# Performance work log

Measured on AMD Instinct MI355X. Metric: run time of the kernel, lower is better.

## Reference

```python
import jax, jax.numpy as jnp
import numpy as np

N_AGENTS = 8
STATE_DIM = 256
EMBED_DIM = 32
BATCH = 65536


def setup_inputs() -> dict:
    key = jax.random.key(0)
    ks = jax.random.split(key, 12)
    s = 1.0 / np.sqrt(STATE_DIM)
    se = 1.0 / np.sqrt(EMBED_DIM)
    return {
        "agent_qs": jax.random.normal(ks[0], (BATCH, N_AGENTS), dtype=jnp.float32),
        "states": jax.random.normal(ks[1], (BATCH, STATE_DIM), dtype=jnp.float32),
        # hyper_w_1: Linear(state_dim, embed_dim * n_agents)
        "w1_W": jax.random.uniform(ks[2], (STATE_DIM, EMBED_DIM * N_AGENTS), jnp.float32, -s, s),
        "w1_b": jax.random.uniform(ks[3], (EMBED_DIM * N_AGENTS,), jnp.float32, -s, s),
        # hyper_w_final: Linear(state_dim, embed_dim)
        "wf_W": jax.random.uniform(ks[4], (STATE_DIM, EMBED_DIM), jnp.float32, -s, s),
        "wf_b": jax.random.uniform(ks[5], (EMBED_DIM,), jnp.float32, -s, s),
        # hyper_b_1: Linear(state_dim, embed_dim)
        "b1_W": jax.random.uniform(ks[6], (STATE_DIM, EMBED_DIM), jnp.float32, -s, s),
        "b1_b": jax.random.uniform(ks[7], (EMBED_DIM,), jnp.float32, -s, s),
        # V: Linear(state_dim, embed_dim) -> ReLU -> Linear(embed_dim, 1)
        "v1_W": jax.random.uniform(ks[8], (STATE_DIM, EMBED_DIM), jnp.float32, -s, s),
        "v1_b": jax.random.uniform(ks[9], (EMBED_DIM,), jnp.float32, -s, s),
        "v2_W": jax.random.uniform(ks[10], (EMBED_DIM, 1), jnp.float32, -se, se),
        "v2_b": jax.random.uniform(ks[11], (1,), jnp.float32, -se, se),
    }


def reference(agent_qs, states, w1_W, w1_b, wf_W, wf_b, b1_W, b1_b, v1_W, v1_b, v2_W, v2_b):
    B = agent_qs.shape[0]
    # hypernet weights (abs for monotonicity)
    w1 = jnp.abs(states @ w1_W + w1_b).reshape(B, N_AGENTS, EMBED_DIM)   # [B, A, E]
    w_final = jnp.abs(states @ wf_W + wf_b)                               # [B, E]
    b1 = states @ b1_W + b1_b                                             # [B, E]
    # hidden = elu(agent_qs^T w1 + b1): [B,1,A] @ [B,A,E] -> [B,E]
    hidden = jax.nn.elu(jnp.einsum("ba,bae->be", agent_qs, w1) + b1)
    # mixed = hidden @ w_final: [B,1,E] @ [B,E,1] -> [B,1]
    mixed = jnp.sum(hidden * w_final, axis=-1, keepdims=True)             # [B, 1]
    # state value V(s)
    state_value = jax.nn.relu(states @ v1_W + v1_b) @ v2_W + v2_b         # [B, 1]
    return mixed + state_value
```

## Files before the change

kernel.cpp:

```cpp
#include <hip/hip_runtime.h>
#include <math.h>


#define NTILES 22
#define KCHUNKS 8
#define CHUNK_I4 1408

typedef __attribute__((ext_vector_type(8))) short short8;
typedef __attribute__((ext_vector_type(4))) float float4v;

__device__ __forceinline__ unsigned short f2b(float f) {
    unsigned int u = __float_as_uint(f);
    u = u + 0x7fffu + ((u >> 16) & 1u);
    return (unsigned short)(u >> 16);
}

__device__ __forceinline__ void gl2lds16(const unsigned short* g, unsigned short* l) {
    __builtin_amdgcn_global_load_lds(
        (const __attribute__((address_space(1))) unsigned int*)g,
        (__attribute__((address_space(3))) unsigned int*)l,
        16, 0, 0);
}

__device__ __forceinline__ float4v ld16_async(const float* p) {
    float4v r;
    asm volatile("global_load_dwordx4 %0, %1, off" : "=v"(r) : "v"(p));
    return r;
}

__global__ void repack_b(const float* __restrict__ w1_W,
                         const float* __restrict__ wf_W,
                         const float* __restrict__ b1_W,
                         const float* __restrict__ v1_W,
                         unsigned short* __restrict__ brep) {
    int idx = blockIdx.x * 256 + threadIdx.x;
    int lane = idx & 63;
    int tt   = idx >> 6;
    int t    = tt % 22;
    int kc   = tt / 22;
    int kbase = kc * 32 + (lane >> 4) * 8;
    int n = t * 16 + (lane & 15);
    short8 frag;
#pragma unroll
    for (int j = 0; j < 8; ++j) {
        int k = kbase + j;
        float val;
        if (n < 256)      val = w1_W[k * 256 + n];
        else if (n < 288) val = wf_W[k * 32 + (n - 256)];
        else if (n < 320) val = b1_W[k * 32 + (n - 288)];
        else              val = v1_W[k * 32 + (n - 320)];
        frag[j] = (short)f2b(val);
    }
    *(short8*)(&brep[idx * 8]) = frag;
}

__global__ void __launch_bounds__(256, 2)
qmix_main(const float* __restrict__ agent_qs,
          const float* __restrict__ states,
          const unsigned short* __restrict__ brep,
          const float* __restrict__ w1_b,
          const float* __restrict__ wf_b,
          const float* __restrict__ b1_b,
          const float* __restrict__ v1_b,
          const float* __restrict__ v2_W,
          const float* __restrict__ v2_b,
          float* __restrict__ out) {
    __shared__ __align__(16) unsigned short wlds[2][NTILES * 64 * 8];

    const int tid  = threadIdx.x;
    const int wave = tid >> 6, lane = tid & 63;
    const int quad = lane >> 4, l16 = lane & 15;
    const int r0 = blockIdx.x * 128 + wave * 32 + l16;
    const float* srow0 = states + (size_t)r0 * 256;
    const float* srow1 = srow0 + 16 * 256;

    float4v st[4];

#define ISSUE_STATES(kcv) do {                                          \
        const float* p0_ = srow0 + (kcv) * 32 + quad * 8;               \
        const float* p1_ = srow1 + (kcv) * 32 + quad * 8;               \
        st[0] = ld16_async(p0_);                                        \
        st[1] = ld16_async(p0_ + 4);                                    \
        st[2] = ld16_async(p1_);                                        \
        st[3] = ld16_async(p1_ + 4);                                    \
    } while (0)

#define ISSUE_DMA(kcv, bufv) do {                                       \
        const unsigned short* src_ = brep + (size_t)(kcv) * CHUNK_I4 * 8; \
        unsigned short* dst_ = wlds[bufv];                              \
        for (int s_ = wave; s_ < NTILES; s_ += 4)                       \
            gl2lds16(src_ + (size_t)(s_ * 64 + lane) * 8, dst_ + s_ * 512); \
    } while (0)

    ISSUE_DMA(0, 0);
    ISSUE_STATES(0);
    ISSUE_DMA(1, 1);

    float4v acc[2][NTILES];
#pragma unroll
    for (int g = 0; g < 2; ++g)
#pragma unroll
        for (int t = 0; t < NTILES; ++t)
#pragma unroll
            for (int q = 0; q < 4; ++q) acc[g][t][q] = 0.f;

#pragma unroll
    for (int kc = 0; kc < KCHUNKS; ++kc) {
        const int buf = kc & 1;

        if (kc == KCHUNKS - 1)
            asm volatile("s_waitcnt vmcnt(0)" ::: "memory");
        else if (wave < 2)
            asm volatile("s_waitcnt vmcnt(6)" ::: "memory");
        else
            asm volatile("s_waitcnt vmcnt(5)" ::: "memory");
        __builtin_amdgcn_sched_barrier(0);
        __builtin_amdgcn_s_barrier();
        __builtin_amdgcn_sched_barrier(0);

        short8 b0, b1;
#pragma unroll
        for (int j = 0; j < 4; ++j) {
            b0[j]     = (short)f2b(st[0][j]);
            b0[4 + j] = (short)f2b(st[1][j]);
            b1[j]     = (short)f2b(st[2][j]);
            b1[4 + j] = (short)f2b(st[3][j]);
        }
        if (kc + 1 < KCHUNKS) ISSUE_STATES(kc + 1);

        const short8* wb = (const short8*)wlds[buf] + lane;
#pragma unroll
        for (int t = 0; t < NTILES; ++t) {
            short8 af = wb[t * 64];
            acc[0][t] = __builtin_amdgcn_mfma_f32_16x16x32_bf16(af, b0, acc[0][t], 0, 0, 0);
            acc[1][t] = __builtin_amdgcn_mfma_f32_16x16x32_bf16(af, b1, acc[1][t], 0, 0, 0);
        }

        if (kc + 2 < KCHUNKS) {
            asm volatile("s_waitcnt lgkmcnt(0)" ::: "memory");
            __builtin_amdgcn_sched_barrier(0);
            __builtin_amdgcn_s_barrier();
            __builtin_amdgcn_sched_barrier(0);
            ISSUE_DMA(kc + 2, buf);
        }
    }

#pragma unroll
    for (int g = 0; g < 2; ++g) {
        const int row = r0 + g * 16;
        float4v q0 = *(const float4v*)(agent_qs + (size_t)row * 8);
        float4v q1 = *(const float4v*)(agent_qs + (size_t)row * 8 + 4);
        float qv[8] = {q0[0], q0[1], q0[2], q0[3], q1[0], q1[1], q1[2], q1[3]};

        float qacc[8], wfv[8], b1v[8], svp = 0.f;
#pragma unroll
        for (int s = 0; s < 8; ++s) qacc[s] = 0.f;

#pragma unroll
        for (int t = 0; t < NTILES; ++t) {
            const float* bptr =
                (t < 16) ? (w1_b + t * 16) :
                (t < 18) ? (wf_b + (t - 16) * 16) :
                (t < 20) ? (b1_b + (t - 18) * 16) : (v1_b + (t - 20) * 16);
            float4v bb = *(const float4v*)(bptr + quad * 4);
            float vb[4];
#pragma unroll
            for (int j = 0; j < 4; ++j) vb[j] = acc[g][t][j] + bb[j];

            if (t < 16) {
                float q = qv[t >> 1];
                int base = (t & 1) * 4;
#pragma unroll
                for (int j = 0; j < 4; ++j) qacc[base + j] += q * fabsf(vb[j]);
            } else if (t < 18) {
                int base = (t - 16) * 4;
#pragma unroll
                for (int j = 0; j < 4; ++j) wfv[base + j] = fabsf(vb[j]);
            } else if (t < 20) {
                int base = (t - 18) * 4;
#pragma unroll
                for (int j = 0; j < 4; ++j) b1v[base + j] = vb[j];
            } else {
                int ebase = (t - 20) * 16 + quad * 4;
#pragma unroll
                for (int j = 0; j < 4; ++j)
                    svp += fmaxf(vb[j], 0.f) * v2_W[ebase + j];
            }
        }

        float mix = 0.f;
#pragma unroll
        for (int s = 0; s < 8; ++s) {
            float h = qacc[s] + b1v[s];
            h = h > 0.f ? h : (__expf(h) - 1.f);
            mix += h * wfv[s];
        }
        float tot = mix + svp;
        tot += __shfl_xor(tot, 16);
        tot += __shfl_xor(tot, 32);
        if (quad == 0) out[row] = tot + v2_b[0];
    }
}

extern "C" void kernel_launch(void* const* d_in, const int* in_sizes, int n_in,
                              void* d_out, int out_size, void* d_ws, size_t ws_size,
                              hipStream_t stream) {
    const float* agent_qs = (const float*)d_in[0];
    const float* states   = (const float*)d_in[1];
    const float* w1_W = (const float*)d_in[2];
    const float* w1_b = (const float*)d_in[3];
    const float* wf_W = (const float*)d_in[4];
    const float* wf_b = (const float*)d_in[5];
    const float* b1_W = (const float*)d_in[6];
    const float* b1_b = (const float*)d_in[7];
    const float* v1_W = (const float*)d_in[8];
    const float* v1_b = (const float*)d_in[9];
    const float* v2_W = (const float*)d_in[10];
    const float* v2_b = (const float*)d_in[11];
    float* out = (float*)d_out;
    unsigned short* brep = (unsigned short*)d_ws;

    repack_b<<<44, 256, 0, stream>>>(w1_W, wf_W, b1_W, v1_W, brep);
    qmix_main<<<512, 256, 0, stream>>>(agent_qs, states, brep,
                                       w1_b, wf_b, b1_b, v1_b, v2_W, v2_b, out);
}
```

Baseline: 127.1 us.

## Split output tiles across wave pairs with 512-thread blocks and LDS reduction

Doubles the block to 512 threads and gives each pair of waves the same 32 rows, with each wave computing half of the 22 N-tiles (11 each). This halves per-thread accumulator registers, so more waves can be resident to hide memory latency. The partial agent-weighted sums from the first half are exchanged through LDS and combined by the second half before the ELU and final reduction. In exchange, each states row is loaded twice (once per wave in the pair), and the epilogue adds extra barriers and an LDS round trip.

```diff
diff --git a/kernel.cpp b/kernel.cpp
--- a/kernel.cpp
+++ b/kernel.cpp
@@ -54,7 +54,7 @@
     *(short8*)(&brep[idx * 8]) = frag;
 }
 
-__global__ void __launch_bounds__(256, 2)
+__global__ void __launch_bounds__(512, 3)
 qmix_main(const float* __restrict__ agent_qs,
           const float* __restrict__ states,
           const unsigned short* __restrict__ brep,
@@ -70,25 +70,26 @@
     const int tid  = threadIdx.x;
     const int wave = tid >> 6, lane = tid & 63;
     const int quad = lane >> 4, l16 = lane & 15;
-    const int r0 = blockIdx.x * 128 + wave * 32 + l16;
-    const float* srow0 = states + (size_t)r0 * 256;
+    const int pair = wave >> 1;
+    const int half = wave & 1;
+    const int tbase = half * 11;
+    const int r0 = blockIdx.x * 128 + pair * 32 + l16;
+    const float* srow0 = states + (size_t)r0 * 256 + quad * 8;
     const float* srow1 = srow0 + 16 * 256;
 
     float4v st[4];
 
 #define ISSUE_STATES(kcv) do {                                          \
-        const float* p0_ = srow0 + (kcv) * 32 + quad * 8;               \
-        const float* p1_ = srow1 + (kcv) * 32 + quad * 8;               \
-        st[0] = ld16_async(p0_);                                        \
-        st[1] = ld16_async(p0_ + 4);                                    \
-        st[2] = ld16_async(p1_);                                        \
-        st[3] = ld16_async(p1_ + 4);                                    \
+        st[0] = ld16_async(srow0 + (kcv) * 32);                         \
+        st[1] = ld16_async(srow0 + (kcv) * 32 + 4);                     \
+        st[2] = ld16_async(srow1 + (kcv) * 32);                         \
+        st[3] = ld16_async(srow1 + (kcv) * 32 + 4);                     \
     } while (0)
 
 #define ISSUE_DMA(kcv, bufv) do {                                       \
         const unsigned short* src_ = brep + (size_t)(kcv) * CHUNK_I4 * 8; \
         unsigned short* dst_ = wlds[bufv];                              \
-        for (int s_ = wave; s_ < NTILES; s_ += 4)                       \
+        for (int s_ = wave; s_ < NTILES; s_ += 8)                       \
             gl2lds16(src_ + (size_t)(s_ * 64 + lane) * 8, dst_ + s_ * 512); \
     } while (0)
 
@@ -96,13 +97,13 @@
     ISSUE_STATES(0);
     ISSUE_DMA(1, 1);
 
-    float4v acc[2][NTILES];
+    float4v acc[2][11];
 #pragma unroll
     for (int g = 0; g < 2; ++g)
 #pragma unroll
-        for (int t = 0; t < NTILES; ++t)
-#pragma unroll
-            for (int q = 0; q < 4; ++q) acc[g][t][q] = 0.f;
+        for (int i = 0; i < 11; ++i)
+#pragma unroll
+            for (int q = 0; q < 4; ++q) acc[g][i][q] = 0.f;
 
 #pragma unroll
     for (int kc = 0; kc < KCHUNKS; ++kc) {
@@ -110,10 +111,10 @@
 
         if (kc == KCHUNKS - 1)
             asm volatile("s_waitcnt vmcnt(0)" ::: "memory");
-        else if (wave < 2)
-            asm volatile("s_waitcnt vmcnt(6)" ::: "memory");
+        else if (wave < 6)
+            asm volatile("s_waitcnt vmcnt(3)" ::: "memory");
         else
-            asm volatile("s_waitcnt vmcnt(5)" ::: "memory");
+            asm volatile("s_waitcnt vmcnt(2)" ::: "memory");
         __builtin_amdgcn_sched_barrier(0);
         __builtin_amdgcn_s_barrier();
         __builtin_amdgcn_sched_barrier(0);
@@ -130,10 +131,10 @@
 
         const short8* wb = (const short8*)wlds[buf] + lane;
 #pragma unroll
-        for (int t = 0; t < NTILES; ++t) {
-            short8 af = wb[t * 64];
-            acc[0][t] = __builtin_amdgcn_mfma_f32_16x16x32_bf16(af, b0, acc[0][t], 0, 0, 0);
-            acc[1][t] = __builtin_amdgcn_mfma_f32_16x16x32_bf16(af, b1, acc[1][t], 0, 0, 0);
+        for (int i = 0; i < 11; ++i) {
+            short8 af = wb[(tbase + i) * 64];
+            acc[0][i] = __builtin_amdgcn_mfma_f32_16x16x32_bf16(af, b0, acc[0][i], 0, 0, 0);
+            acc[1][i] = __builtin_amdgcn_mfma_f32_16x16x32_bf16(af, b1, acc[1][i], 0, 0, 0);
         }
 
         if (kc + 2 < KCHUNKS) {
@@ -145,6 +146,9 @@
         }
     }
 
+    __syncthreads();
+    float* scr = (float*)wlds;
+
 #pragma unroll
     for (int g = 0; g < 2; ++g) {
         const int row = r0 + g * 16;
@@ -154,10 +158,11 @@
 
         float qacc[8], wfv[8], b1v[8], svp = 0.f;
 #pragma unroll
-        for (int s = 0; s < 8; ++s) qacc[s] = 0.f;
-
-#pragma unroll
-        for (int t = 0; t < NTILES; ++t) {
+        for (int s = 0; s < 8; ++s) { qacc[s] = 0.f; wfv[s] = 0.f; b1v[s] = 0.f; }
+
+#pragma unroll
+        for (int i = 0; i < 11; ++i) {
+            const int t = tbase + i;
             const float* bptr =
                 (t < 16) ? (w1_b + t * 16) :
                 (t < 18) ? (wf_b + (t - 16) * 16) :
@@ -165,7 +170,7 @@
             float4v bb = *(const float4v*)(bptr + quad * 4);
             float vb[4];
 #pragma unroll
-            for (int j = 0; j < 4; ++j) vb[j] = acc[g][t][j] + bb[j];
+            for (int j = 0; j < 4; ++j) vb[j] = acc[g][i][j] + bb[j];
 
             if (t < 16) {
                 float q = qv[t >> 1];
@@ -188,17 +193,28 @@
             }
         }
 
-        float mix = 0.f;
-#pragma unroll
-        for (int s = 0; s < 8; ++s) {
-            float h = qacc[s] + b1v[s];
-            h = h > 0.f ? h : (__expf(h) - 1.f);
-            mix += h * wfv[s];
-        }
-        float tot = mix + svp;
-        tot += __shfl_xor(tot, 16);
-        tot += __shfl_xor(tot, 32);
-        if (quad == 0) out[row] = tot + v2_b[0];
+        float* reg = scr + (size_t)(pair * 2 + g) * 512 + lane * 8;
+        if (half == 0) {
+            *(float4v*)(reg)     = *(float4v*)(qacc);
+            *(float4v*)(reg + 4) = *(float4v*)(qacc + 4);
+        }
+        __syncthreads();
+        if (half == 1) {
+            float4v pa = *(const float4v*)(reg);
+            float4v pb = *(const float4v*)(reg + 4);
+            float mix = 0.f;
+#pragma unroll
+            for (int s = 0; s < 8; ++s) {
+                float qs = qacc[s] + ((s < 4) ? pa[s] : pb[s - 4]);
+                float h = qs + b1v[s];
+                h = h > 0.f ? h : (__expf(h) - 1.f);
+                mix += h * wfv[s];
+            }
+            float tot = mix + svp;
+            tot += __shfl_xor(tot, 16);
+            tot += __shfl_xor(tot, 32);
+            if (quad == 0) out[row] = tot + v2_b[0];
+        }
     }
 }
 
@@ -221,6 +237,6 @@
     unsigned short* brep = (unsigned short*)d_ws;
 
     repack_b<<<44, 256, 0, stream>>>(w1_W, wf_W, b1_W, v1_W, brep);
-    qmix_main<<<512, 256, 0, stream>>>(agent_qs, states, brep,
+    qmix_main<<<512, 512, 0, stream>>>(agent_qs, states, brep,
                                        w1_b, wf_b, b1_b, v1_b, v2_W, v2_b, out);
 }
```

After: 147.8 us. +16.3%, slower.
